# Kernel optimization log

Measured on AMD Instinct MI355X. Metric: run time of the kernel, lower is better.

The kernel has to match this reference:

```python
import jax, jax.numpy as jnp
import numpy as np

D_MODEL = 1024
N_HEADS = 16
D_HEAD = D_MODEL // N_HEADS
ROPE_BASE = 10000.0


def setup_inputs() -> dict:
    key = jax.random.key(0)
    k1, k2, k3, k4, k5 = jax.random.split(key, 5)
    std = 0.02 / np.sqrt(2 * 12)  # scaled_xavier with n_layers=12
    x = jax.random.normal(k1, (2, 2048, D_MODEL), dtype=jnp.float32)
    qkv_w = jax.random.normal(k2, (3 * D_MODEL, D_MODEL), dtype=jnp.float32) * std
    qkv_b = jnp.zeros((3 * D_MODEL,), dtype=jnp.float32)
    proj_w = jax.random.normal(k3, (D_MODEL, D_MODEL), dtype=jnp.float32) * std
    proj_b = jnp.zeros((D_MODEL,), dtype=jnp.float32)
    return {"x": x, "qkv_w": qkv_w, "qkv_b": qkv_b, "proj_w": proj_w, "proj_b": proj_b}


def _rope_cos_sin(seq_len, dtype):
    inv_freq = 1.0 / (ROPE_BASE ** (jnp.arange(0, D_HEAD, 2, dtype=jnp.float32) / D_HEAD))
    t = jnp.arange(seq_len, dtype=jnp.float32)
    freqs = jnp.einsum("t,d->td", t, inv_freq)          # [S, Dh/2]
    freqs = jnp.concatenate([freqs, freqs], axis=-1)      # [S, Dh]
    return jnp.cos(freqs).astype(dtype), jnp.sin(freqs).astype(dtype)


def _rotate_half(x):
    x1, x2 = jnp.split(x, 2, axis=-1)
    return jnp.concatenate([-x2, x1], axis=-1)


def reference(x, qkv_w, qkv_b, proj_w, proj_b):
    B, S, D = x.shape
    H, Dh = N_HEADS, D_HEAD
    scale = 1.0 / np.sqrt(Dh)

    qkv = x @ qkv_w.T + qkv_b                              # [B, S, 3D]
    qkv = qkv.reshape(B, S, 3, H, Dh)
    q = jnp.transpose(qkv[:, :, 0], (0, 2, 1, 3))          # [B, H, S, Dh]
    k = jnp.transpose(qkv[:, :, 1], (0, 2, 1, 3))
    v = jnp.transpose(qkv[:, :, 2], (0, 2, 1, 3))

    cos, sin = _rope_cos_sin(S, x.dtype)                   # [S, Dh]
    q = q * cos + _rotate_half(q) * sin
    k = k * cos + _rotate_half(k) * sin

    scores = jnp.einsum("bhsd,bhtd->bhst", q, k) * scale   # [B, H, S, S]
    causal = jnp.triu(jnp.ones((S, S), dtype=bool), k=1)
    neg = jnp.finfo(scores.dtype).min
    scores = jnp.where(causal[None, None], neg, scores)

    probs = jax.nn.softmax(scores, axis=-1)
    ctx = jnp.einsum("bhst,bhtd->bhsd", probs, v)          # [B, H, S, Dh]
    out = jnp.transpose(ctx, (0, 2, 1, 3)).reshape(B, S, D)
    out = out @ proj_w.T + proj_b
    return out
```

## Files before the change

kernel.cpp:

```cpp
#include <hip/hip_runtime.h>
#include <hip/hip_bf16.h>

#define BATCH 2
#define SEQ   2048
#define DMODEL 1024
#define NHEADS 16
#define DHEAD  64
#define MTOT   (BATCH * SEQ)
#define QKSTR  2048

typedef __attribute__((ext_vector_type(8))) short bf16x8;
typedef __attribute__((ext_vector_type(4))) short bf16x4;
typedef __attribute__((ext_vector_type(4))) float f32x4;

__device__ __forceinline__ void glds16(const void* g, void* l)
{
    __builtin_amdgcn_global_load_lds(
        (const __attribute__((address_space(1))) unsigned int*)g,
        (__attribute__((address_space(3))) unsigned int*)l, 16, 0, 0);
}

__device__ __forceinline__ unsigned cvt_pk_bf16(float lo, float hi)
{
    unsigned r;
    asm("v_cvt_pk_bf16_f32 %0, %1, %2" : "=v"(r) : "v"(lo), "v"(hi));
    return r;
}

__device__ __forceinline__ float fast_exp2(float x)
{
    float r;
    asm("v_exp_f32 %0, %1" : "=v"(r) : "v"(x));
    return r;
}

__global__ void cast_all_kernel(
    const float* __restrict__ a, __hip_bfloat16* __restrict__ oa, int na4,
    const float* __restrict__ b, __hip_bfloat16* __restrict__ ob, int nb4,
    const float* __restrict__ c, __hip_bfloat16* __restrict__ oc, int nc4)
{
    int i = blockIdx.x * blockDim.x + threadIdx.x;
    const float* src; __hip_bfloat16* dst; int j = i;
    if (j < na4) { src = a; dst = oa; }
    else {
        j -= na4;
        if (j < nb4) { src = b; dst = ob; }
        else {
            j -= nb4;
            if (j >= nc4) return;
            src = c; dst = oc;
        }
    }
    float4 v = ((const float4*)src)[j];
    __hip_bfloat16 tmp[4];
    tmp[0] = __float2bfloat16(v.x);
    tmp[1] = __float2bfloat16(v.y);
    tmp[2] = __float2bfloat16(v.z);
    tmp[3] = __float2bfloat16(v.w);
    *(uint2*)(dst + 4 * (size_t)j) = *(const uint2*)tmp;
}

#define GBK 64

__device__ __forceinline__ void store_out(float* p, float v) { *p = v; }
__device__ __forceinline__ void store_out(__hip_bfloat16* p, float v) { *p = __float2bfloat16(v); }

template <typename OutT, int MODE, int TM, int TN, int MINW>
__global__ __launch_bounds__(256, MINW) void gemm_bias_kernel(
    const __hip_bfloat16* __restrict__ A, const __hip_bfloat16* __restrict__ W,
    const float* __restrict__ bias, OutT* __restrict__ out,
    __hip_bfloat16* __restrict__ vtg,
    int M, int N, int K)
{
    const int MI = TM / 32;
    const int NI = TN / 32;
    const int bm = blockIdx.x * TM;
    const int bn = blockIdx.y * TN;
    const int tid = threadIdx.x;
    const int wave = tid >> 6;
    const int lane = tid & 63;
    const int quad = lane >> 4;
    const int l16 = lane & 15;
    const int wm = (wave & 1) * (TM / 2);
    const int wn = (wave >> 1) * (TN / 2);

    __shared__ __hip_bfloat16 As[TM * GBK];
    __shared__ __hip_bfloat16 Bs[TN * GBK];

    f32x4 acc[MI][NI] = {};

    const int srow = lane >> 3;
    const int gc8 = (((lane & 7) ^ srow)) * 8;

    for (int kt = 0; kt < K; kt += GBK) {
#pragma unroll
        for (int t = 0; t < MI; t++) {
            int i = wave * MI + t;
            glds16(A + (size_t)(bm + i * 8 + srow) * K + kt + gc8, As + i * 512);
        }
#pragma unroll
        for (int t = 0; t < NI; t++) {
            int i = wave * NI + t;
            glds16(W + (size_t)(bn + i * 8 + srow) * K + kt + gc8, Bs + i * 512);
        }
        __syncthreads();

#pragma unroll
        for (int kk = 0; kk < 2; kk++) {
            bf16x8 af[MI], bfr[NI];
#pragma unroll
            for (int i = 0; i < MI; i++) {
                int ra = wm + i * 16 + l16;
                af[i] = *(const bf16x8*)(As + ra * 64 + (((kk << 2) + quad) ^ (ra & 7)) * 8);
            }
#pragma unroll
            for (int i = 0; i < NI; i++) {
                int rb = wn + i * 16 + l16;
                bfr[i] = *(const bf16x8*)(Bs + rb * 64 + (((kk << 2) + quad) ^ (rb & 7)) * 8);
            }
#pragma unroll
            for (int mi = 0; mi < MI; mi++)
#pragma unroll
                for (int ni = 0; ni < NI; ni++)
                    acc[mi][ni] = __builtin_amdgcn_mfma_f32_16x16x32_bf16(
                        af[mi], bfr[ni], acc[mi][ni], 0, 0, 0);
        }
        __syncthreads();
    }

    if (MODE == 1 && (bn + wn) < 2 * DMODEL) {
#pragma unroll
        for (int ni = 0; ni < 2; ni++) {
            int col = bn + wn + ni * 16 + l16;
            int i32 = col & 31;
            float invf = exp2f(-13.287712379549449f * (float)i32 * (1.0f / 32.0f));
            float b1 = bias[col], b2 = bias[col + 32];
#pragma unroll
            for (int mi = 0; mi < MI; mi++) {
#pragma unroll
                for (int r = 0; r < 4; r++) {
                    int row = bm + wm + mi * 16 + quad * 4 + r;
                    int s = row & (SEQ - 1);
                    float ang = (float)s * invf;
                    float sn, cs;
                    __sincosf(ang, &sn, &cs);
                    float x1 = acc[mi][ni][r] + b1;
                    float x2 = acc[mi][ni + 2][r] + b2;
                    store_out(&out[(size_t)row * QKSTR + col], x1 * cs - x2 * sn);
                    store_out(&out[(size_t)row * QKSTR + col + 32], x2 * cs + x1 * sn);
                }
            }
        }
    } else if (MODE == 1) {
#pragma unroll
        for (int ni = 0; ni < NI; ni++) {
            int colg = bn + wn + ni * 16 + l16;
            int vcol = colg - 2 * DMODEL;
            int hh = vcol >> 6, dh = vcol & 63;
            float bv = bias[colg];
#pragma unroll
            for (int mi = 0; mi < MI; mi++) {
                int row0 = bm + wm + mi * 16 + quad * 4;
                int bb = row0 >> 11;
                int ss = row0 & (SEQ - 1);
                __hip_bfloat16 tmp[4];
#pragma unroll
                for (int r = 0; r < 4; r++)
                    tmp[r] = __float2bfloat16(acc[mi][ni][r] + bv);
                *(uint2*)(vtg + (((size_t)bb * NHEADS + hh) * DHEAD + dh) * SEQ + ss) =
                    *(uint2*)tmp;
            }
        }
    } else {
#pragma unroll
        for (int mi = 0; mi < MI; mi++)
#pragma unroll
            for (int ni = 0; ni < NI; ni++) {
                int col = bn + wn + ni * 16 + l16;
                float bv = bias[col];
#pragma unroll
                for (int r = 0; r < 4; r++) {
                    int row = bm + wm + mi * 16 + quad * 4 + r;
                    store_out(&out[(size_t)row * N + col], acc[mi][ni][r] + bv);
                }
            }
    }
}

__global__ __launch_bounds__(256, 3) void flash_attn_mfma_kernel(
    const __hip_bfloat16* __restrict__ qkb,
    const __hip_bfloat16* __restrict__ vtg,
    __hip_bfloat16* __restrict__ ctx)
{
    const int bh = blockIdx.x;
    const int b = bh >> 4, h = bh & 15;
    const int qt = 31 - blockIdx.y;
    const int tid = threadIdx.x;
    const int w = tid >> 6;
    const int lane = tid & 63;
    const int quad = lane >> 4;
    const int l16 = lane & 15;

    __shared__ alignas(16) __hip_bfloat16 smem[24576];
    __hip_bfloat16* const ksb = smem;
    __hip_bfloat16* const vtb = smem + 12288;

    const __hip_bfloat16* qbase = qkb + (size_t)b * SEQ * QKSTR + h * DHEAD;
    const __hip_bfloat16* kbase = qbase + DMODEL;
    const __hip_bfloat16* vbase = vtg + (size_t)bh * DHEAD * SEQ;

    bf16x8 qf[4][2];
#pragma unroll
    for (int tq = 0; tq < 4; tq++) {
        const __hip_bfloat16* qr =
            qbase + (size_t)(qt * 64 + tq * 16 + l16) * QKSTR;
        qf[tq][0] = *(const bf16x8*)(qr + quad * 8);
        qf[tq][1] = *(const bf16x8*)(qr + 32 + quad * 8);
    }

    const int srow = lane >> 3;
    const int gc8 = ((lane & 7) ^ srow) * 8;
    const __hip_bfloat16* kg = kbase + (size_t)(w * 16 + srow) * QKSTR + gc8;
    const __hip_bfloat16* vg = vbase + (size_t)(w * 16 + srow) * SEQ + gc8;

    const int xr = l16 & 7;
    const int foK0 = (w * 16 + l16) * 64 + ((quad ^ xr) << 3);
    const int foK1 = (w * 16 + l16) * 64 + (((4 + quad) ^ xr) << 3);
    int vb[4];
#pragma unroll
    for (int dt = 0; dt < 4; dt++)
        vb[dt] = (dt * 16 + l16) * 64 +
                 ((((w << 1) + (quad >> 1)) ^ xr) << 3) + ((quad & 1) << 2);

    const short ov = (l16 == 0) ? (short)0x3F80 : (short)0;
    const bf16x4 ones4 = {ov, ov, ov, ov};

    f32x4 oacc[4][4] = {};
    f32x4 lacc[4] = {};

    auto stage = [&](int t, int buf) {
        const __hip_bfloat16* kt_ = kg + (size_t)t * 64 * QKSTR;
        const __hip_bfloat16* vt_ = vg + t * 64;
        glds16(kt_,             ksb + buf * 4096 + w * 1024);
        glds16(kt_ + 8 * QKSTR, ksb + buf * 4096 + w * 1024 + 512);
        glds16(vt_,             vtb + buf * 4096 + w * 1024);
        glds16(vt_ + 8 * SEQ,   vtb + buf * 4096 + w * 1024 + 512);
    };

    stage(0, 0);
    stage(1, 1);

    int cur = 0;
    for (int jt = 0; jt <= qt; jt++) {
        if (jt < qt) asm volatile("s_waitcnt vmcnt(4)" ::: "memory");
        else         asm volatile("s_waitcnt vmcnt(0)" ::: "memory");
        __builtin_amdgcn_s_barrier();
        __builtin_amdgcn_sched_barrier(0);

        if (jt + 2 <= qt) {
            int nb = cur + 2; if (nb >= 3) nb -= 3;
            stage(jt + 2, nb);
        }
        const __hip_bfloat16* ks = ksb + cur * 4096;
        const __hip_bfloat16* vs = vtb + cur * 4096;

        bf16x8 ka0 = *(const bf16x8*)(ks + foK0);
        bf16x8 ka1 = *(const bf16x8*)(ks + foK1);
        f32x4 s4[4] = {};
        __builtin_amdgcn_s_setprio(1);
#pragma unroll
        for (int tq = 0; tq < 4; tq++)
            s4[tq] = __builtin_amdgcn_mfma_f32_16x16x32_bf16(
                ka0, qf[tq][0], s4[tq], 0, 0, 0);
#pragma unroll
        for (int tq = 0; tq < 4; tq++)
            s4[tq] = __builtin_amdgcn_mfma_f32_16x16x32_bf16(
                ka1, qf[tq][1], s4[tq], 0, 0, 0);
        __builtin_amdgcn_s_setprio(0);

        const bool diag = (jt == qt);
        bf16x4 pa[4];
#pragma unroll
        for (int tq = 0; tq < 4; tq++) {
            float p0 = fast_exp2(s4[tq][0] * 0.1803368801f);
            float p1 = fast_exp2(s4[tq][1] * 0.1803368801f);
            float p2 = fast_exp2(s4[tq][2] * 0.1803368801f);
            float p3 = fast_exp2(s4[tq][3] * 0.1803368801f);
            if (diag) {
                int k0 = w * 16 + quad * 4;
                int qq = tq * 16 + l16;
                p0 = (k0 + 0 <= qq) ? p0 : 0.f;
                p1 = (k0 + 1 <= qq) ? p1 : 0.f;
                p2 = (k0 + 2 <= qq) ? p2 : 0.f;
                p3 = (k0 + 3 <= qq) ? p3 : 0.f;
            }
            union { unsigned u[2]; bf16x4 v; } pu;
            pu.u[0] = cvt_pk_bf16(p0, p1);
            pu.u[1] = cvt_pk_bf16(p2, p3);
            pa[tq] = pu.v;
        }

        bf16x4 vf0 = *(const bf16x4*)(vs + vb[0]);
        bf16x4 vf1 = *(const bf16x4*)(vs + vb[1]);
        bf16x4 vf2 = *(const bf16x4*)(vs + vb[2]);
        bf16x4 vf3 = *(const bf16x4*)(vs + vb[3]);
        __builtin_amdgcn_s_setprio(1);
#pragma unroll
        for (int tq = 0; tq < 4; tq++) {
            oacc[tq][0] = __builtin_amdgcn_mfma_f32_16x16x16bf16_1k(
                pa[tq], vf0, oacc[tq][0], 0, 0, 0);
            oacc[tq][1] = __builtin_amdgcn_mfma_f32_16x16x16bf16_1k(
                pa[tq], vf1, oacc[tq][1], 0, 0, 0);
            oacc[tq][2] = __builtin_amdgcn_mfma_f32_16x16x16bf16_1k(
                pa[tq], vf2, oacc[tq][2], 0, 0, 0);
            oacc[tq][3] = __builtin_amdgcn_mfma_f32_16x16x16bf16_1k(
                pa[tq], vf3, oacc[tq][3], 0, 0, 0);
            lacc[tq] = __builtin_amdgcn_mfma_f32_16x16x16bf16_1k(
                pa[tq], ones4, lacc[tq], 0, 0, 0);
        }
        __builtin_amdgcn_s_setprio(0);

        cur = cur + 1; if (cur >= 3) cur -= 3;
    }

    __syncthreads();
    f32x4* const osh = (f32x4*)smem;
    f32x4* const lsh = (f32x4*)(smem + 16384);

    if (l16 == 0) {
#pragma unroll
        for (int tq = 0; tq < 4; tq++)
            lsh[(w * 4 + tq) * 4 + quad] = lacc[tq];
    }
    __syncthreads();
    f32x4 lt = lsh[(0 * 4 + w) * 4 + quad];
#pragma unroll
    for (int src = 1; src < 4; src++)
        lt += lsh[(src * 4 + w) * 4 + quad];
    f32x4 ilv;
#pragma unroll
    for (int r = 0; r < 4; r++) ilv[r] = 1.0f / lt[r];

#pragma unroll
    for (int p = 0; p < 2; p++) {
        if (p) __syncthreads();
#pragma unroll
        for (int tq = 0; tq < 4; tq++)
#pragma unroll
            for (int d = 0; d < 2; d++)
                osh[((w * 4 + tq) * 2 + d) * 64 + lane] = oacc[tq][p * 2 + d];
        __syncthreads();
#pragma unroll
        for (int d = 0; d < 2; d++) {
            f32x4 os = osh[((0 * 4 + w) * 2 + d) * 64 + lane];
#pragma unroll
            for (int src = 1; src < 4; src++)
                os += osh[((src * 4 + w) * 2 + d) * 64 + lane];
            const int dh = (p * 2 + d) * 16 + l16;
#pragma unroll
            for (int r = 0; r < 4; r++) {
                int qg = qt * 64 + w * 16 + quad * 4 + r;
                ctx[(((size_t)b * SEQ + qg) * NHEADS + h) * DHEAD + dh] =
                    __float2bfloat16(os[r] * ilv[r]);
            }
        }
    }
}

extern "C" void kernel_launch(void* const* d_in, const int* in_sizes, int n_in,
                              void* d_out, int out_size, void* d_ws, size_t ws_size,
                              hipStream_t stream)
{
    const float* x      = (const float*)d_in[0];
    const float* qkv_w  = (const float*)d_in[1];
    const float* qkv_b  = (const float*)d_in[2];
    const float* proj_w = (const float*)d_in[3];
    const float* proj_b = (const float*)d_in[4];
    float* out = (float*)d_out;

    char* w = (char*)d_ws;
    __hip_bfloat16* qkb = (__hip_bfloat16*)w;  w += (size_t)MTOT * QKSTR * 2;
    __hip_bfloat16* vtg = (__hip_bfloat16*)w;  w += (size_t)MTOT * DMODEL * 2;
    __hip_bfloat16* ctx = (__hip_bfloat16*)w;  w += (size_t)MTOT * DMODEL * 2;
    __hip_bfloat16* xb  = (__hip_bfloat16*)w;  w += (size_t)MTOT * DMODEL * 2;
    __hip_bfloat16* wqk = (__hip_bfloat16*)w;  w += (size_t)3 * DMODEL * DMODEL * 2;
    __hip_bfloat16* wpr = (__hip_bfloat16*)w;

    const int na4 = MTOT * DMODEL / 4;
    const int nb4 = 3 * DMODEL * DMODEL / 4;
    const int nc4 = DMODEL * DMODEL / 4;

    cast_all_kernel<<<(na4 + nb4 + nc4 + 255) / 256, 256, 0, stream>>>(
        x, xb, na4, qkv_w, wqk, nb4, proj_w, wpr, nc4);

    gemm_bias_kernel<__hip_bfloat16, 1, 128, 128, 3>
        <<<dim3(MTOT / 128, (3 * DMODEL) / 128), 256, 0, stream>>>(
        xb, wqk, qkv_b, qkb, vtg, MTOT, 3 * DMODEL, DMODEL);

    flash_attn_mfma_kernel<<<dim3(BATCH * NHEADS, 32), 256, 0, stream>>>(qkb, vtg, ctx);

    gemm_bias_kernel<float, 0, 64, 128, 6>
        <<<dim3(MTOT / 64, DMODEL / 128), 256, 0, stream>>>(
        ctx, wpr, proj_b, out, nullptr, MTOT, DMODEL, DMODEL);
}
```

Baseline: 166.8 us.

## Process two query tiles per attention block with 8 waves sharing K/V staging

The flash attention kernel now uses 512-thread blocks covering 128 query rows (two 64-row groups of 4 waves each) that share the same staged K/V tiles in LDS. Each wave loads half as much per stage, which halves K/V global traffic per query row. The grid is flattened to 512 blocks and ordered heaviest-first. The cost is that the lower query group sits idle on the final K tile while still taking part in barriers, and fewer, larger blocks may reduce occupancy and load-balance flexibility.

```diff
diff --git a/kernel.cpp b/kernel.cpp
--- a/kernel.cpp
+++ b/kernel.cpp
@@ -187,19 +187,22 @@
     }
 }
 
-__global__ __launch_bounds__(256, 3) void flash_attn_mfma_kernel(
+__global__ __launch_bounds__(512, 2) void flash_attn_mfma_kernel(
     const __hip_bfloat16* __restrict__ qkb,
     const __hip_bfloat16* __restrict__ vtg,
     __hip_bfloat16* __restrict__ ctx)
 {
-    const int bh = blockIdx.x;
+    const int idx = blockIdx.x;
+    const int bh = idx & 31;
+    const int qt2 = 15 - (idx >> 5);
     const int b = bh >> 4, h = bh & 15;
-    const int qt = 31 - blockIdx.y;
     const int tid = threadIdx.x;
     const int w = tid >> 6;
     const int lane = tid & 63;
     const int quad = lane >> 4;
     const int l16 = lane & 15;
+    const int kw = w & 3;
+    const int qg = w >> 2;
 
     __shared__ alignas(16) __hip_bfloat16 smem[24576];
     __hip_bfloat16* const ksb = smem;
@@ -213,24 +216,24 @@
 #pragma unroll
     for (int tq = 0; tq < 4; tq++) {
         const __hip_bfloat16* qr =
-            qbase + (size_t)(qt * 64 + tq * 16 + l16) * QKSTR;
+            qbase + (size_t)(qt2 * 128 + qg * 64 + tq * 16 + l16) * QKSTR;
         qf[tq][0] = *(const bf16x8*)(qr + quad * 8);
         qf[tq][1] = *(const bf16x8*)(qr + 32 + quad * 8);
     }
 
     const int srow = lane >> 3;
     const int gc8 = ((lane & 7) ^ srow) * 8;
-    const __hip_bfloat16* kg = kbase + (size_t)(w * 16 + srow) * QKSTR + gc8;
-    const __hip_bfloat16* vg = vbase + (size_t)(w * 16 + srow) * SEQ + gc8;
+    const __hip_bfloat16* kg = kbase + (size_t)(w * 8 + srow) * QKSTR + gc8;
+    const __hip_bfloat16* vg = vbase + (size_t)(w * 8 + srow) * SEQ + gc8;
 
     const int xr = l16 & 7;
-    const int foK0 = (w * 16 + l16) * 64 + ((quad ^ xr) << 3);
-    const int foK1 = (w * 16 + l16) * 64 + (((4 + quad) ^ xr) << 3);
+    const int foK0 = (kw * 16 + l16) * 64 + ((quad ^ xr) << 3);
+    const int foK1 = (kw * 16 + l16) * 64 + (((4 + quad) ^ xr) << 3);
     int vb[4];
 #pragma unroll
     for (int dt = 0; dt < 4; dt++)
         vb[dt] = (dt * 16 + l16) * 64 +
-                 ((((w << 1) + (quad >> 1)) ^ xr) << 3) + ((quad & 1) << 2);
+                 ((((kw << 1) + (quad >> 1)) ^ xr) << 3) + ((quad & 1) << 2);
 
     const short ov = (l16 == 0) ? (short)0x3F80 : (short)0;
     const bf16x4 ones4 = {ov, ov, ov, ov};
@@ -239,87 +242,87 @@
     f32x4 lacc[4] = {};
 
     auto stage = [&](int t, int buf) {
-        const __hip_bfloat16* kt_ = kg + (size_t)t * 64 * QKSTR;
-        const __hip_bfloat16* vt_ = vg + t * 64;
-        glds16(kt_,             ksb + buf * 4096 + w * 1024);
-        glds16(kt_ + 8 * QKSTR, ksb + buf * 4096 + w * 1024 + 512);
-        glds16(vt_,             vtb + buf * 4096 + w * 1024);
-        glds16(vt_ + 8 * SEQ,   vtb + buf * 4096 + w * 1024 + 512);
+        glds16(kg + (size_t)t * 64 * QKSTR, ksb + buf * 4096 + w * 512);
+        glds16(vg + t * 64,                 vtb + buf * 4096 + w * 512);
     };
+
+    const int nit = 2 * qt2 + 2;
+    const int jd = 2 * qt2 + qg;
 
     stage(0, 0);
     stage(1, 1);
 
     int cur = 0;
-    for (int jt = 0; jt <= qt; jt++) {
-        if (jt < qt) asm volatile("s_waitcnt vmcnt(4)" ::: "memory");
-        else         asm volatile("s_waitcnt vmcnt(0)" ::: "memory");
+    for (int jt = 0; jt < nit; jt++) {
+        if (jt < nit - 1) asm volatile("s_waitcnt vmcnt(2)" ::: "memory");
+        else              asm volatile("s_waitcnt vmcnt(0)" ::: "memory");
         __builtin_amdgcn_s_barrier();
         __builtin_amdgcn_sched_barrier(0);
 
-        if (jt + 2 <= qt) {
+        if (jt + 2 < nit) {
             int nb = cur + 2; if (nb >= 3) nb -= 3;
             stage(jt + 2, nb);
         }
-        const __hip_bfloat16* ks = ksb + cur * 4096;
-        const __hip_bfloat16* vs = vtb + cur * 4096;
-
-        bf16x8 ka0 = *(const bf16x8*)(ks + foK0);
-        bf16x8 ka1 = *(const bf16x8*)(ks + foK1);
-        f32x4 s4[4] = {};
-        __builtin_amdgcn_s_setprio(1);
-#pragma unroll
-        for (int tq = 0; tq < 4; tq++)
-            s4[tq] = __builtin_amdgcn_mfma_f32_16x16x32_bf16(
-                ka0, qf[tq][0], s4[tq], 0, 0, 0);
-#pragma unroll
-        for (int tq = 0; tq < 4; tq++)
-            s4[tq] = __builtin_amdgcn_mfma_f32_16x16x32_bf16(
-                ka1, qf[tq][1], s4[tq], 0, 0, 0);
-        __builtin_amdgcn_s_setprio(0);
-
-        const bool diag = (jt == qt);
-        bf16x4 pa[4];
-#pragma unroll
-        for (int tq = 0; tq < 4; tq++) {
-            float p0 = fast_exp2(s4[tq][0] * 0.1803368801f);
-            float p1 = fast_exp2(s4[tq][1] * 0.1803368801f);
-            float p2 = fast_exp2(s4[tq][2] * 0.1803368801f);
-            float p3 = fast_exp2(s4[tq][3] * 0.1803368801f);
-            if (diag) {
-                int k0 = w * 16 + quad * 4;
-                int qq = tq * 16 + l16;
-                p0 = (k0 + 0 <= qq) ? p0 : 0.f;
-                p1 = (k0 + 1 <= qq) ? p1 : 0.f;
-                p2 = (k0 + 2 <= qq) ? p2 : 0.f;
-                p3 = (k0 + 3 <= qq) ? p3 : 0.f;
-            }
-            union { unsigned u[2]; bf16x4 v; } pu;
-            pu.u[0] = cvt_pk_bf16(p0, p1);
-            pu.u[1] = cvt_pk_bf16(p2, p3);
-            pa[tq] = pu.v;
-        }
-
-        bf16x4 vf0 = *(const bf16x4*)(vs + vb[0]);
-        bf16x4 vf1 = *(const bf16x4*)(vs + vb[1]);
-        bf16x4 vf2 = *(const bf16x4*)(vs + vb[2]);
-        bf16x4 vf3 = *(const bf16x4*)(vs + vb[3]);
-        __builtin_amdgcn_s_setprio(1);
-#pragma unroll
-        for (int tq = 0; tq < 4; tq++) {
-            oacc[tq][0] = __builtin_amdgcn_mfma_f32_16x16x16bf16_1k(
-                pa[tq], vf0, oacc[tq][0], 0, 0, 0);
-            oacc[tq][1] = __builtin_amdgcn_mfma_f32_16x16x16bf16_1k(
-                pa[tq], vf1, oacc[tq][1], 0, 0, 0);
-            oacc[tq][2] = __builtin_amdgcn_mfma_f32_16x16x16bf16_1k(
-                pa[tq], vf2, oacc[tq][2], 0, 0, 0);
-            oacc[tq][3] = __builtin_amdgcn_mfma_f32_16x16x16bf16_1k(
-                pa[tq], vf3, oacc[tq][3], 0, 0, 0);
-            lacc[tq] = __builtin_amdgcn_mfma_f32_16x16x16bf16_1k(
-                pa[tq], ones4, lacc[tq], 0, 0, 0);
-        }
-        __builtin_amdgcn_s_setprio(0);
-
+        if (jt <= jd) {
+            const __hip_bfloat16* ks = ksb + cur * 4096;
+            const __hip_bfloat16* vs = vtb + cur * 4096;
+
+            bf16x8 ka0 = *(const bf16x8*)(ks + foK0);
+            bf16x8 ka1 = *(const bf16x8*)(ks + foK1);
+            f32x4 s4[4] = {};
+            __builtin_amdgcn_s_setprio(1);
+#pragma unroll
+            for (int tq = 0; tq < 4; tq++)
+                s4[tq] = __builtin_amdgcn_mfma_f32_16x16x32_bf16(
+                    ka0, qf[tq][0], s4[tq], 0, 0, 0);
+#pragma unroll
+            for (int tq = 0; tq < 4; tq++)
+                s4[tq] = __builtin_amdgcn_mfma_f32_16x16x32_bf16(
+                    ka1, qf[tq][1], s4[tq], 0, 0, 0);
+            __builtin_amdgcn_s_setprio(0);
+
+            const bool diag = (jt == jd);
+            bf16x4 pa[4];
+#pragma unroll
+            for (int tq = 0; tq < 4; tq++) {
+                float p0 = fast_exp2(s4[tq][0] * 0.1803368801f);
+                float p1 = fast_exp2(s4[tq][1] * 0.1803368801f);
+                float p2 = fast_exp2(s4[tq][2] * 0.1803368801f);
+                float p3 = fast_exp2(s4[tq][3] * 0.1803368801f);
+                if (diag) {
+                    int k0 = kw * 16 + quad * 4;
+                    int qq = tq * 16 + l16;
+                    p0 = (k0 + 0 <= qq) ? p0 : 0.f;
+                    p1 = (k0 + 1 <= qq) ? p1 : 0.f;
+                    p2 = (k0 + 2 <= qq) ? p2 : 0.f;
+                    p3 = (k0 + 3 <= qq) ? p3 : 0.f;
+                }
+                union { unsigned u[2]; bf16x4 v; } pu;
+                pu.u[0] = cvt_pk_bf16(p0, p1);
+                pu.u[1] = cvt_pk_bf16(p2, p3);
+                pa[tq] = pu.v;
+            }
+
+            bf16x4 vf0 = *(const bf16x4*)(vs + vb[0]);
+            bf16x4 vf1 = *(const bf16x4*)(vs + vb[1]);
+            bf16x4 vf2 = *(const bf16x4*)(vs + vb[2]);
+            bf16x4 vf3 = *(const bf16x4*)(vs + vb[3]);
+            __builtin_amdgcn_s_setprio(1);
+#pragma unroll
+            for (int tq = 0; tq < 4; tq++) {
+                oacc[tq][0] = __builtin_amdgcn_mfma_f32_16x16x16bf16_1k(
+                    pa[tq], vf0, oacc[tq][0], 0, 0, 0);
+                oacc[tq][1] = __builtin_amdgcn_mfma_f32_16x16x16bf16_1k(
+                    pa[tq], vf1, oacc[tq][1], 0, 0, 0);
+                oacc[tq][2] = __builtin_amdgcn_mfma_f32_16x16x16bf16_1k(
+                    pa[tq], vf2, oacc[tq][2], 0, 0, 0);
+                oacc[tq][3] = __builtin_amdgcn_mfma_f32_16x16x16bf16_1k(
+                    pa[tq], vf3, oacc[tq][3], 0, 0, 0);
+                lacc[tq] = __builtin_amdgcn_mfma_f32_16x16x16bf16_1k(
+                    pa[tq], ones4, lacc[tq], 0, 0, 0);
+            }
+            __builtin_amdgcn_s_setprio(0);
+        }
         cur = cur + 1; if (cur >= 3) cur -= 3;
     }
 
@@ -330,39 +333,34 @@
     if (l16 == 0) {
 #pragma unroll
         for (int tq = 0; tq < 4; tq++)
-            lsh[(w * 4 + tq) * 4 + quad] = lacc[tq];
+            lsh[((qg * 4 + kw) * 4 + tq) * 4 + quad] = lacc[tq];
     }
     __syncthreads();
-    f32x4 lt = lsh[(0 * 4 + w) * 4 + quad];
+    f32x4 lt = lsh[((qg * 4 + 0) * 4 + kw) * 4 + quad];
 #pragma unroll
     for (int src = 1; src < 4; src++)
-        lt += lsh[(src * 4 + w) * 4 + quad];
+        lt += lsh[((qg * 4 + src) * 4 + kw) * 4 + quad];
     f32x4 ilv;
 #pragma unroll
     for (int r = 0; r < 4; r++) ilv[r] = 1.0f / lt[r];
 
 #pragma unroll
-    for (int p = 0; p < 2; p++) {
-        if (p) __syncthreads();
+    for (int dt = 0; dt < 4; dt++) {
+        __syncthreads();
 #pragma unroll
         for (int tq = 0; tq < 4; tq++)
-#pragma unroll
-            for (int d = 0; d < 2; d++)
-                osh[((w * 4 + tq) * 2 + d) * 64 + lane] = oacc[tq][p * 2 + d];
+            osh[((qg * 4 + kw) * 4 + tq) * 64 + lane] = oacc[tq][dt];
         __syncthreads();
-#pragma unroll
-        for (int d = 0; d < 2; d++) {
-            f32x4 os = osh[((0 * 4 + w) * 2 + d) * 64 + lane];
-#pragma unroll
-            for (int src = 1; src < 4; src++)
-                os += osh[((src * 4 + w) * 2 + d) * 64 + lane];
-            const int dh = (p * 2 + d) * 16 + l16;
-#pragma unroll
-            for (int r = 0; r < 4; r++) {
-                int qg = qt * 64 + w * 16 + quad * 4 + r;
-                ctx[(((size_t)b * SEQ + qg) * NHEADS + h) * DHEAD + dh] =
-                    __float2bfloat16(os[r] * ilv[r]);
-            }
+        f32x4 os = osh[((qg * 4 + 0) * 4 + kw) * 64 + lane];
+#pragma unroll
+        for (int src = 1; src < 4; src++)
+            os += osh[((qg * 4 + src) * 4 + kw) * 64 + lane];
+        const int dh = dt * 16 + l16;
+#pragma unroll
+        for (int r = 0; r < 4; r++) {
+            int qg_row = qt2 * 128 + qg * 64 + kw * 16 + quad * 4 + r;
+            ctx[(((size_t)b * SEQ + qg_row) * NHEADS + h) * DHEAD + dh] =
+                __float2bfloat16(os[r] * ilv[r]);
         }
     }
 }
@@ -397,7 +395,7 @@
         <<<dim3(MTOT / 128, (3 * DMODEL) / 128), 256, 0, stream>>>(
         xb, wqk, qkv_b, qkb, vtg, MTOT, 3 * DMODEL, DMODEL);
 
-    flash_attn_mfma_kernel<<<dim3(BATCH * NHEADS, 32), 256, 0, stream>>>(qkb, vtg, ctx);
+    flash_attn_mfma_kernel<<<512, 512, 0, stream>>>(qkb, vtg, ctx);
 
     gemm_bias_kernel<float, 0, 64, 128, 6>
         <<<dim3(MTOT / 64, DMODEL / 128), 256, 0, stream>>>(
```

Result: no change. 168.1 us (+0.8%).
